# Kernel optimization log

Measured on AMD Instinct MI355X. Metric: run time of the kernel, lower is better.

## Reference

```python
import jax, jax.numpy as jnp
import numpy as np

B, S, FEAT, DK = 128, 2048, 512, 64

def setup_inputs() -> dict:
    key = jax.random.key(0)
    k1, k2, k3, k4, k5 = jax.random.split(key, 5)
    input_k = jax.random.normal(k1, (B, S, FEAT), dtype=jnp.float32)
    input_q = jax.random.normal(k2, (B, FEAT), dtype=jnp.float32)
    context_len = jax.random.randint(k3, (B,), 0, S + 1, dtype=jnp.int32)
    # Linear weights stored as [in, out] so y = x @ W
    W_K = jax.random.normal(k4, (FEAT, DK), dtype=jnp.float32) / np.sqrt(FEAT)
    W_Q = jax.random.normal(k5, (FEAT, DK), dtype=jnp.float32) / np.sqrt(FEAT)
    return {"input_k": input_k, "input_q": input_q, "context_len": context_len,
            "W_K": W_K, "W_Q": W_Q}

def reference(input_k, input_q, context_len, W_K, W_Q):
    # K: [B,S,dk], q: [B,dk]
    K = jnp.einsum('bsf,fd->bsd', input_k, W_K)
    q = input_q @ W_Q
    scores = jnp.einsum('bd,bsd->bs', q, K)  # [B,S] (n_heads=1, no scaling in original)
    mask = jnp.arange(S)[None, :] < context_len[:, None]  # [B,S]
    attn = jax.nn.softmax(jnp.where(mask, scores, -1e30), axis=-1)  # [B,S]
    context = jnp.einsum('bs,bsf->bf', attn, input_k)  # [B,FEAT]
    # length==0 rows produce zeros in the original
    context = jnp.where((context_len > 0)[:, None], context, 0.0)
    return context
```

## Files before the change

### kernel.cpp

```cpp
#include <hip/hip_runtime.h>
#include <math.h>

#define B_    128
#define S_    2048
#define FEAT_ 512
#define DK_   64
#define NSPLIT 32
#define CHUNK  (S_ / NSPLIT)

typedef float f32x4 __attribute__((ext_vector_type(4)));

#define SBAR() __builtin_amdgcn_sched_barrier(0)

__device__ __forceinline__ void ld4(f32x4& d, const float* p) {
  asm volatile("global_load_dwordx4 %0, %1, off" : "=v"(d) : "v"(p) : "memory");
}
__device__ __forceinline__ void ld4o(f32x4& d, const float* p) {
  asm volatile("global_load_dwordx4 %0, %1, off offset:1024"
               : "=v"(d) : "v"(p) : "memory");
}
#define VWAIT(N)                                              \
  do {                                                        \
    asm volatile("s_waitcnt vmcnt(" #N ")" ::: "memory");     \
    SBAR();                                                   \
  } while (0)

#define ISSUE4(d0, d1, d2, d3, d4, d5, d6, d7, srow)                \
  do {                                                              \
    const float* r_ = base + (size_t)(srow) * FEAT_ + lane * 4;     \
    ld4(d0, r_);              ld4o(d1, r_);                         \
    ld4(d2, r_ + 4 * FEAT_);  ld4o(d3, r_ + 4 * FEAT_);             \
    ld4(d4, r_ + 8 * FEAT_);  ld4o(d5, r_ + 8 * FEAT_);             \
    ld4(d6, r_ + 12 * FEAT_); ld4o(d7, r_ + 12 * FEAT_);            \
    SBAR();                                                         \
  } while (0)

__device__ __forceinline__ float dot8(f32x4 x0, f32x4 x1, f32x4 v0, f32x4 v1) {
  float p = x0[0] * v0[0];
  p = fmaf(x0[1], v0[1], p);
  p = fmaf(x0[2], v0[2], p);
  p = fmaf(x0[3], v0[3], p);
  p = fmaf(x1[0], v1[0], p);
  p = fmaf(x1[1], v1[1], p);
  p = fmaf(x1[2], v1[2], p);
  p = fmaf(x1[3], v1[3], p);
  return p;
}

__device__ __forceinline__ float wredsum(float p) {
#pragma unroll
  for (int off = 32; off; off >>= 1) p += __shfl_xor(p, off, 64);
  return p;
}

__device__ __forceinline__ void compute4(
    f32x4 x0, f32x4 x1, f32x4 x2, f32x4 x3,
    f32x4 x4, f32x4 x5, f32x4 x6, f32x4 x7,
    f32x4 v0, f32x4 v1, float& m, float& l, f32x4& a0, f32x4& a1) {
  float p0 = dot8(x0, x1, v0, v1);
  float p1 = dot8(x2, x3, v0, v1);
  float p2 = dot8(x4, x5, v0, v1);
  float p3 = dot8(x6, x7, v0, v1);
  p0 = wredsum(p0);
  p1 = wredsum(p1);
  p2 = wredsum(p2);
  p3 = wredsum(p3);
  float mn = fmaxf(fmaxf(fmaxf(p0, p1), fmaxf(p2, p3)), m);
  float sc = __expf(m - mn);
  float w0 = __expf(p0 - mn), w1 = __expf(p1 - mn);
  float w2 = __expf(p2 - mn), w3 = __expf(p3 - mn);
  l = fmaf(l, sc, (w0 + w1) + (w2 + w3));
#pragma unroll
  for (int j = 0; j < 4; ++j) {
    a0[j] = fmaf(w0, x0[j],
            fmaf(w1, x2[j], fmaf(w2, x4[j], fmaf(w3, x6[j], a0[j] * sc))));
    a1[j] = fmaf(w0, x1[j],
            fmaf(w1, x3[j], fmaf(w2, x5[j], fmaf(w3, x7[j], a1[j] * sc))));
  }
  m = mn;
}

__global__ __launch_bounds__(256) void qv_kernel(
    const float* __restrict__ input_q, const float* __restrict__ W_Q,
    const float* __restrict__ W_K, float* __restrict__ v) {
  int b = blockIdx.x;
  int tid = threadIdx.x;
  __shared__ float xq[FEAT_];
  __shared__ float part[4][DK_];
  __shared__ float qs[DK_];
  for (int f = tid; f < FEAT_; f += 256) xq[f] = input_q[b * FEAT_ + f];
  __syncthreads();
  {
    int d = tid & 63, c = tid >> 6;
    float s = 0.f;
    int f0 = c * 128;
    for (int f = f0; f < f0 + 128; ++f) s = fmaf(xq[f], W_Q[f * DK_ + d], s);
    part[c][d] = s;
  }
  __syncthreads();
  if (tid < DK_)
    qs[tid] = part[0][tid] + part[1][tid] + part[2][tid] + part[3][tid];
  __syncthreads();
  for (int f = tid; f < FEAT_; f += 256) {
    const f32x4* wk = (const f32x4*)(W_K + f * DK_);
    float s = 0.f;
#pragma unroll
    for (int d4 = 0; d4 < DK_ / 4; ++d4) {
      f32x4 w = wk[d4];
      s = fmaf(w[0], qs[d4 * 4 + 0], s);
      s = fmaf(w[1], qs[d4 * 4 + 1], s);
      s = fmaf(w[2], qs[d4 * 4 + 2], s);
      s = fmaf(w[3], qs[d4 * 4 + 3], s);
    }
    v[b * FEAT_ + f] = s;
  }
}

__global__ __launch_bounds__(256) void pass_kernel(
    const float* __restrict__ input_k, const int* __restrict__ ctx,
    const float* __restrict__ v, float* __restrict__ pm,
    float* __restrict__ pl, float* __restrict__ pacc) {
  int split = blockIdx.x;
  int b = blockIdx.y;
  int L = ctx[b];
  int s0 = split * CHUNK;
  int tid = threadIdx.x, wave = tid >> 6, lane = tid & 63;
  int idx = b * NSPLIT + split;

  if (s0 >= L) {
    if (tid == 0) { pm[idx] = -INFINITY; pl[idx] = 0.f; }
    return;
  }

  const float* vb = v + b * FEAT_ + lane * 4;
  f32x4 v0, v1;
  ld4(v0, vb);
  ld4o(v1, vb);
  VWAIT(0);

  float m = -INFINITY, l = 0.f;
  f32x4 a0 = {0.f, 0.f, 0.f, 0.f};
  f32x4 a1 = {0.f, 0.f, 0.f, 0.f};

  const float* base = input_k + (size_t)b * S_ * FEAT_;
  int sb = s0 + wave;

  if (L >= s0 + CHUNK) {
    f32x4 c0, c1, c2, c3, c4, c5, c6, c7;
    f32x4 n0, n1, n2, n3, n4, n5, n6, n7;
    ISSUE4(c0, c1, c2, c3, c4, c5, c6, c7, sb);
    ISSUE4(n0, n1, n2, n3, n4, n5, n6, n7, sb + 16);
    VWAIT(8);
    compute4(c0, c1, c2, c3, c4, c5, c6, c7, v0, v1, m, l, a0, a1);
    ISSUE4(c0, c1, c2, c3, c4, c5, c6, c7, sb + 32);
    VWAIT(8);
    compute4(n0, n1, n2, n3, n4, n5, n6, n7, v0, v1, m, l, a0, a1);
    ISSUE4(n0, n1, n2, n3, n4, n5, n6, n7, sb + 48);
    VWAIT(8);
    compute4(c0, c1, c2, c3, c4, c5, c6, c7, v0, v1, m, l, a0, a1);
    VWAIT(0);
    compute4(n0, n1, n2, n3, n4, n5, n6, n7, v0, v1, m, l, a0, a1);
  } else {
    int s1 = L;
    int s = sb;
    for (; s + 12 < s1; s += 16) {
      const float* r_ = base + (size_t)s * FEAT_ + lane * 4;
      f32x4 x0 = *(const f32x4*)(r_);
      f32x4 x1 = *(const f32x4*)(r_ + 256);
      f32x4 x2 = *(const f32x4*)(r_ + 4 * FEAT_);
      f32x4 x3 = *(const f32x4*)(r_ + 4 * FEAT_ + 256);
      f32x4 x4 = *(const f32x4*)(r_ + 8 * FEAT_);
      f32x4 x5 = *(const f32x4*)(r_ + 8 * FEAT_ + 256);
      f32x4 x6 = *(const f32x4*)(r_ + 12 * FEAT_);
      f32x4 x7 = *(const f32x4*)(r_ + 12 * FEAT_ + 256);
      compute4(x0, x1, x2, x3, x4, x5, x6, x7, v0, v1, m, l, a0, a1);
    }
    for (; s < s1; s += 4) {
      const float* r_ = base + (size_t)s * FEAT_ + lane * 4;
      f32x4 x0 = *(const f32x4*)(r_);
      f32x4 x1 = *(const f32x4*)(r_ + 256);
      float p = wredsum(dot8(x0, x1, v0, v1));
      float mn = fmaxf(m, p);
      float sc = __expf(m - mn);
      float w = __expf(p - mn);
      l = fmaf(l, sc, w);
#pragma unroll
      for (int j = 0; j < 4; ++j) {
        a0[j] = fmaf(w, x0[j], a0[j] * sc);
        a1[j] = fmaf(w, x1[j], a1[j] * sc);
      }
      m = mn;
    }
  }

  __shared__ float sm[4], sl[4];
  __shared__ float sa[4][FEAT_];
  if (lane == 0) { sm[wave] = m; sl[wave] = l; }
  *(f32x4*)&sa[wave][lane * 4] = a0;
  *(f32x4*)&sa[wave][256 + lane * 4] = a1;
  __syncthreads();

  float M = fmaxf(fmaxf(sm[0], sm[1]), fmaxf(sm[2], sm[3]));
  float e0 = __expf(sm[0] - M), e1 = __expf(sm[1] - M);
  float e2 = __expf(sm[2] - M), e3 = __expf(sm[3] - M);
  if (tid == 0) {
    pm[idx] = M;
    pl[idx] = e0 * sl[0] + e1 * sl[1] + e2 * sl[2] + e3 * sl[3];
  }
  for (int f = tid; f < FEAT_; f += 256)
    pacc[(size_t)idx * FEAT_ + f] =
        e0 * sa[0][f] + e1 * sa[1][f] + e2 * sa[2][f] + e3 * sa[3][f];
}

__global__ __launch_bounds__(256) void combine_kernel(
    const float* __restrict__ pm, const float* __restrict__ pl,
    const float* __restrict__ pacc, float* __restrict__ out) {
  int b = blockIdx.x;
  int tid = threadIdx.x;
  __shared__ float e[NSPLIT];
  __shared__ float inv_s;
  if (tid < NSPLIT) {
    float mi = pm[b * NSPLIT + tid];
    float M = mi;
#pragma unroll
    for (int off = 16; off; off >>= 1) M = fmaxf(M, __shfl_xor(M, off, 64));
    float ei = (M == -INFINITY) ? 0.f : __expf(mi - M);
    e[tid] = ei;
    float lw = ei * pl[b * NSPLIT + tid];
#pragma unroll
    for (int off = 16; off; off >>= 1) lw += __shfl_xor(lw, off, 64);
    if (tid == 0) inv_s = (lw > 0.f) ? 1.f / lw : 0.f;
  }
  __syncthreads();
  float inv = inv_s;
  for (int f = tid; f < FEAT_; f += 256) {
    float s = 0.f;
    for (int i = 0; i < NSPLIT; ++i)
      if (e[i] > 0.f)
        s = fmaf(e[i], pacc[((size_t)(b * NSPLIT + i)) * FEAT_ + f], s);
    out[b * FEAT_ + f] = s * inv;
  }
}

extern "C" void kernel_launch(void* const* d_in, const int* in_sizes, int n_in,
                              void* d_out, int out_size, void* d_ws, size_t ws_size,
                              hipStream_t stream) {
  const float* input_k = (const float*)d_in[0];
  const float* input_q = (const float*)d_in[1];
  const int*   ctx     = (const int*)d_in[2];
  const float* W_K     = (const float*)d_in[3];
  const float* W_Q     = (const float*)d_in[4];
  float* out = (float*)d_out;

  char* ws = (char*)d_ws;
  float* v    = (float*)ws;
  float* pm   = (float*)(ws + (size_t)B_ * FEAT_ * sizeof(float));
  float* pl   = pm + B_ * NSPLIT;
  float* pacc = pl + B_ * NSPLIT;

  qv_kernel<<<B_, 256, 0, stream>>>(input_q, W_Q, W_K, v);
  pass_kernel<<<dim3(NSPLIT, B_), 256, 0, stream>>>(input_k, ctx, v, pm, pl, pacc);
  combine_kernel<<<B_, 256, 0, stream>>>(pm, pl, pacc, out);
}
```

Before: 76.06 us.

## Stage key rows through LDS with async global_load_lds double buffering

The full-chunk path now streams key rows into a per-wave double-buffered LDS staging area using global_load_lds instead of inline-asm register loads. Each wave reads two rows at a time from LDS, computes the online softmax update, and refills the buffer while the math runs. The tail path also drops from four to two rows per iteration, and the staging buffer is reused for the cross-wave reduction. The aim is to lower VGPR pressure and overlap memory with compute, at the cost of an extra LDS round trip and more lgkm waits per row pair.

```diff
diff --git a/kernel.cpp b/kernel.cpp
--- a/kernel.cpp
+++ b/kernel.cpp
@@ -11,29 +11,22 @@
 typedef float f32x4 __attribute__((ext_vector_type(4)));
 
 #define SBAR() __builtin_amdgcn_sched_barrier(0)
-
-__device__ __forceinline__ void ld4(f32x4& d, const float* p) {
-  asm volatile("global_load_dwordx4 %0, %1, off" : "=v"(d) : "v"(p) : "memory");
-}
-__device__ __forceinline__ void ld4o(f32x4& d, const float* p) {
-  asm volatile("global_load_dwordx4 %0, %1, off offset:1024"
-               : "=v"(d) : "v"(p) : "memory");
-}
-#define VWAIT(N)                                              \
-  do {                                                        \
-    asm volatile("s_waitcnt vmcnt(" #N ")" ::: "memory");     \
-    SBAR();                                                   \
+#define VWAIT(N)                                                  \
+  do {                                                            \
+    asm volatile("s_waitcnt vmcnt(" #N ")" ::: "memory");         \
+    SBAR();                                                       \
   } while (0)
-
-#define ISSUE4(d0, d1, d2, d3, d4, d5, d6, d7, srow)                \
-  do {                                                              \
-    const float* r_ = base + (size_t)(srow) * FEAT_ + lane * 4;     \
-    ld4(d0, r_);              ld4o(d1, r_);                         \
-    ld4(d2, r_ + 4 * FEAT_);  ld4o(d3, r_ + 4 * FEAT_);             \
-    ld4(d4, r_ + 8 * FEAT_);  ld4o(d5, r_ + 8 * FEAT_);             \
-    ld4(d6, r_ + 12 * FEAT_); ld4o(d7, r_ + 12 * FEAT_);            \
-    SBAR();                                                         \
+#define LWAIT()                                                   \
+  do {                                                            \
+    asm volatile("s_waitcnt lgkmcnt(0)" ::: "memory");            \
+    SBAR();                                                       \
   } while (0)
+
+__device__ __forceinline__ void glds16(const float* g, float* l) {
+  __builtin_amdgcn_global_load_lds(
+      (const __attribute__((address_space(1))) void*)g,
+      (__attribute__((address_space(3))) void*)l, 16, 0, 0);
+}
 
 __device__ __forceinline__ float dot8(f32x4 x0, f32x4 x1, f32x4 v0, f32x4 v1) {
   float p = x0[0] * v0[0];
@@ -53,29 +46,22 @@
   return p;
 }
 
-__device__ __forceinline__ void compute4(
-    f32x4 x0, f32x4 x1, f32x4 x2, f32x4 x3,
-    f32x4 x4, f32x4 x5, f32x4 x6, f32x4 x7,
+__device__ __forceinline__ void math2(
+    f32x4 xA0, f32x4 xA1, f32x4 xB0, f32x4 xB1,
     f32x4 v0, f32x4 v1, float& m, float& l, f32x4& a0, f32x4& a1) {
-  float p0 = dot8(x0, x1, v0, v1);
-  float p1 = dot8(x2, x3, v0, v1);
-  float p2 = dot8(x4, x5, v0, v1);
-  float p3 = dot8(x6, x7, v0, v1);
+  float p0 = dot8(xA0, xA1, v0, v1);
+  float p1 = dot8(xB0, xB1, v0, v1);
   p0 = wredsum(p0);
   p1 = wredsum(p1);
-  p2 = wredsum(p2);
-  p3 = wredsum(p3);
-  float mn = fmaxf(fmaxf(fmaxf(p0, p1), fmaxf(p2, p3)), m);
+  float mn = fmaxf(m, fmaxf(p0, p1));
   float sc = __expf(m - mn);
-  float w0 = __expf(p0 - mn), w1 = __expf(p1 - mn);
-  float w2 = __expf(p2 - mn), w3 = __expf(p3 - mn);
-  l = fmaf(l, sc, (w0 + w1) + (w2 + w3));
+  float w0 = __expf(p0 - mn);
+  float w1 = __expf(p1 - mn);
+  l = fmaf(l, sc, w0 + w1);
 #pragma unroll
   for (int j = 0; j < 4; ++j) {
-    a0[j] = fmaf(w0, x0[j],
-            fmaf(w1, x2[j], fmaf(w2, x4[j], fmaf(w3, x6[j], a0[j] * sc))));
-    a1[j] = fmaf(w0, x1[j],
-            fmaf(w1, x3[j], fmaf(w2, x5[j], fmaf(w3, x7[j], a1[j] * sc))));
+    a0[j] = fmaf(w0, xA0[j], fmaf(w1, xB0[j], a0[j] * sc));
+    a1[j] = fmaf(w0, xA1[j], fmaf(w1, xB1[j], a1[j] * sc));
   }
   m = mn;
 }
@@ -120,6 +106,9 @@
     const float* __restrict__ input_k, const int* __restrict__ ctx,
     const float* __restrict__ v, float* __restrict__ pm,
     float* __restrict__ pl, float* __restrict__ pacc) {
+  __shared__ __align__(16) float stage[4][2][1024];
+  __shared__ float sm[4], sl[4];
+
   int split = blockIdx.x;
   int b = blockIdx.y;
   int L = ctx[b];
@@ -133,49 +122,73 @@
   }
 
   const float* vb = v + b * FEAT_ + lane * 4;
-  f32x4 v0, v1;
-  ld4(v0, vb);
-  ld4o(v1, vb);
-  VWAIT(0);
+  f32x4 v0 = *(const f32x4*)vb;
+  f32x4 v1 = *(const f32x4*)(vb + 256);
 
   float m = -INFINITY, l = 0.f;
   f32x4 a0 = {0.f, 0.f, 0.f, 0.f};
   f32x4 a1 = {0.f, 0.f, 0.f, 0.f};
 
   const float* base = input_k + (size_t)b * S_ * FEAT_;
-  int sb = s0 + wave;
+  float* st0 = &stage[wave][0][0];
+  float* st1 = &stage[wave][1][0];
 
   if (L >= s0 + CHUNK) {
-    f32x4 c0, c1, c2, c3, c4, c5, c6, c7;
-    f32x4 n0, n1, n2, n3, n4, n5, n6, n7;
-    ISSUE4(c0, c1, c2, c3, c4, c5, c6, c7, sb);
-    ISSUE4(n0, n1, n2, n3, n4, n5, n6, n7, sb + 16);
-    VWAIT(8);
-    compute4(c0, c1, c2, c3, c4, c5, c6, c7, v0, v1, m, l, a0, a1);
-    ISSUE4(c0, c1, c2, c3, c4, c5, c6, c7, sb + 32);
-    VWAIT(8);
-    compute4(n0, n1, n2, n3, n4, n5, n6, n7, v0, v1, m, l, a0, a1);
-    ISSUE4(n0, n1, n2, n3, n4, n5, n6, n7, sb + 48);
-    VWAIT(8);
-    compute4(c0, c1, c2, c3, c4, c5, c6, c7, v0, v1, m, l, a0, a1);
+    const float* rb = base + (size_t)(s0 + wave) * FEAT_ + lane * 4;
+#define GISSUE(g_, st_)                                     \
+    do {                                                    \
+      const float* gp_ = rb + (size_t)4096 * (g_);          \
+      glds16(gp_,        (st_));                            \
+      glds16(gp_ + 256,  (st_) + 256);                      \
+      glds16(gp_ + 2048, (st_) + 512);                      \
+      glds16(gp_ + 2304, (st_) + 768);                      \
+    } while (0)
+#define LOAD2(st_, xA0, xA1, xB0, xB1)                      \
+    do {                                                    \
+      const f32x4* p_ = (const f32x4*)(st_) + lane;         \
+      xA0 = p_[0];                                          \
+      xA1 = p_[64];                                         \
+      xB0 = p_[128];                                        \
+      xB1 = p_[192];                                        \
+    } while (0)
+
+    GISSUE(0, st0);
+    GISSUE(1, st1);
     VWAIT(0);
-    compute4(n0, n1, n2, n3, n4, n5, n6, n7, v0, v1, m, l, a0, a1);
+#pragma unroll
+    for (int g = 0; g < 6; ++g) {
+      float* cur = (g & 1) ? st1 : st0;
+      f32x4 xA0, xA1, xB0, xB1;
+      LOAD2(cur, xA0, xA1, xB0, xB1);
+      LWAIT();
+      GISSUE(g + 2, cur);
+      math2(xA0, xA1, xB0, xB1, v0, v1, m, l, a0, a1);
+      VWAIT(4);
+    }
+    {
+      f32x4 xA0, xA1, xB0, xB1;
+      LOAD2(st0, xA0, xA1, xB0, xB1);
+      math2(xA0, xA1, xB0, xB1, v0, v1, m, l, a0, a1);
+    }
+    VWAIT(0);
+    {
+      f32x4 xA0, xA1, xB0, xB1;
+      LOAD2(st1, xA0, xA1, xB0, xB1);
+      math2(xA0, xA1, xB0, xB1, v0, v1, m, l, a0, a1);
+    }
+#undef GISSUE
+#undef LOAD2
   } else {
-    int s1 = L;
-    int s = sb;
-    for (; s + 12 < s1; s += 16) {
+    int s = s0 + wave;
+    for (; s + 4 < L; s += 8) {
       const float* r_ = base + (size_t)s * FEAT_ + lane * 4;
-      f32x4 x0 = *(const f32x4*)(r_);
-      f32x4 x1 = *(const f32x4*)(r_ + 256);
-      f32x4 x2 = *(const f32x4*)(r_ + 4 * FEAT_);
-      f32x4 x3 = *(const f32x4*)(r_ + 4 * FEAT_ + 256);
-      f32x4 x4 = *(const f32x4*)(r_ + 8 * FEAT_);
-      f32x4 x5 = *(const f32x4*)(r_ + 8 * FEAT_ + 256);
-      f32x4 x6 = *(const f32x4*)(r_ + 12 * FEAT_);
-      f32x4 x7 = *(const f32x4*)(r_ + 12 * FEAT_ + 256);
-      compute4(x0, x1, x2, x3, x4, x5, x6, x7, v0, v1, m, l, a0, a1);
-    }
-    for (; s < s1; s += 4) {
+      f32x4 xA0 = *(const f32x4*)(r_);
+      f32x4 xA1 = *(const f32x4*)(r_ + 256);
+      f32x4 xB0 = *(const f32x4*)(r_ + 4 * FEAT_);
+      f32x4 xB1 = *(const f32x4*)(r_ + 4 * FEAT_ + 256);
+      math2(xA0, xA1, xB0, xB1, v0, v1, m, l, a0, a1);
+    }
+    if (s < L) {
       const float* r_ = base + (size_t)s * FEAT_ + lane * 4;
       f32x4 x0 = *(const f32x4*)(r_);
       f32x4 x1 = *(const f32x4*)(r_ + 256);
@@ -193,11 +206,12 @@
     }
   }
 
-  __shared__ float sm[4], sl[4];
-  __shared__ float sa[4][FEAT_];
   if (lane == 0) { sm[wave] = m; sl[wave] = l; }
-  *(f32x4*)&sa[wave][lane * 4] = a0;
-  *(f32x4*)&sa[wave][256 + lane * 4] = a1;
+  {
+    f32x4* sw = (f32x4*)&stage[wave][0][0];
+    sw[lane] = a0;
+    sw[64 + lane] = a1;
+  }
   __syncthreads();
 
   float M = fmaxf(fmaxf(sm[0], sm[1]), fmaxf(sm[2], sm[3]));
@@ -209,7 +223,8 @@
   }
   for (int f = tid; f < FEAT_; f += 256)
     pacc[(size_t)idx * FEAT_ + f] =
-        e0 * sa[0][f] + e1 * sa[1][f] + e2 * sa[2][f] + e3 * sa[3][f];
+        e0 * stage[0][0][f] + e1 * stage[1][0][f] +
+        e2 * stage[2][0][f] + e3 * stage[3][0][f];
 }
 
 __global__ __launch_bounds__(256) void combine_kernel(
```

Result: slower. 78.16 us (+2.8%).

## Interleave sequence rows across splits instead of contiguous chunks per split

Applied to the files above, without the earlier changes.

Each split block now takes rows split, split+NSPLIT, split+2*NSPLIT, ... instead of a contiguous CHUNK of rows. This balances work across splits when context lengths are ragged, so no split carries a full chunk while others idle. The hand-written inline-asm double-buffered load pipeline is removed in favour of a plain compiler-scheduled loop. Strided row access loses contiguity between rows inside a block, and the explicit memory-latency overlap is gone.

```diff
diff --git a/kernel.cpp b/kernel.cpp
--- a/kernel.cpp
+++ b/kernel.cpp
@@ -6,34 +6,9 @@
 #define FEAT_ 512
 #define DK_   64
 #define NSPLIT 32
-#define CHUNK  (S_ / NSPLIT)
+#define RSTRIDE (NSPLIT * FEAT_)
 
 typedef float f32x4 __attribute__((ext_vector_type(4)));
-
-#define SBAR() __builtin_amdgcn_sched_barrier(0)
-
-__device__ __forceinline__ void ld4(f32x4& d, const float* p) {
-  asm volatile("global_load_dwordx4 %0, %1, off" : "=v"(d) : "v"(p) : "memory");
-}
-__device__ __forceinline__ void ld4o(f32x4& d, const float* p) {
-  asm volatile("global_load_dwordx4 %0, %1, off offset:1024"
-               : "=v"(d) : "v"(p) : "memory");
-}
-#define VWAIT(N)                                              \
-  do {                                                        \
-    asm volatile("s_waitcnt vmcnt(" #N ")" ::: "memory");     \
-    SBAR();                                                   \
-  } while (0)
-
-#define ISSUE4(d0, d1, d2, d3, d4, d5, d6, d7, srow)                \
-  do {                                                              \
-    const float* r_ = base + (size_t)(srow) * FEAT_ + lane * 4;     \
-    ld4(d0, r_);              ld4o(d1, r_);                         \
-    ld4(d2, r_ + 4 * FEAT_);  ld4o(d3, r_ + 4 * FEAT_);             \
-    ld4(d4, r_ + 8 * FEAT_);  ld4o(d5, r_ + 8 * FEAT_);             \
-    ld4(d6, r_ + 12 * FEAT_); ld4o(d7, r_ + 12 * FEAT_);            \
-    SBAR();                                                         \
-  } while (0)
 
 __device__ __forceinline__ float dot8(f32x4 x0, f32x4 x1, f32x4 v0, f32x4 v1) {
   float p = x0[0] * v0[0];
@@ -53,33 +28,6 @@
   return p;
 }
 
-__device__ __forceinline__ void compute4(
-    f32x4 x0, f32x4 x1, f32x4 x2, f32x4 x3,
-    f32x4 x4, f32x4 x5, f32x4 x6, f32x4 x7,
-    f32x4 v0, f32x4 v1, float& m, float& l, f32x4& a0, f32x4& a1) {
-  float p0 = dot8(x0, x1, v0, v1);
-  float p1 = dot8(x2, x3, v0, v1);
-  float p2 = dot8(x4, x5, v0, v1);
-  float p3 = dot8(x6, x7, v0, v1);
-  p0 = wredsum(p0);
-  p1 = wredsum(p1);
-  p2 = wredsum(p2);
-  p3 = wredsum(p3);
-  float mn = fmaxf(fmaxf(fmaxf(p0, p1), fmaxf(p2, p3)), m);
-  float sc = __expf(m - mn);
-  float w0 = __expf(p0 - mn), w1 = __expf(p1 - mn);
-  float w2 = __expf(p2 - mn), w3 = __expf(p3 - mn);
-  l = fmaf(l, sc, (w0 + w1) + (w2 + w3));
-#pragma unroll
-  for (int j = 0; j < 4; ++j) {
-    a0[j] = fmaf(w0, x0[j],
-            fmaf(w1, x2[j], fmaf(w2, x4[j], fmaf(w3, x6[j], a0[j] * sc))));
-    a1[j] = fmaf(w0, x1[j],
-            fmaf(w1, x3[j], fmaf(w2, x5[j], fmaf(w3, x7[j], a1[j] * sc))));
-  }
-  m = mn;
-}
-
 __global__ __launch_bounds__(256) void qv_kernel(
     const float* __restrict__ input_q, const float* __restrict__ W_Q,
     const float* __restrict__ W_K, float* __restrict__ v) {
@@ -123,74 +71,74 @@
   int split = blockIdx.x;
   int b = blockIdx.y;
   int L = ctx[b];
-  int s0 = split * CHUNK;
   int tid = threadIdx.x, wave = tid >> 6, lane = tid & 63;
   int idx = b * NSPLIT + split;
 
-  if (s0 >= L) {
+  if (split >= L) {
     if (tid == 0) { pm[idx] = -INFINITY; pl[idx] = 0.f; }
     return;
   }
+  int nt = (L - split + NSPLIT - 1) / NSPLIT;
 
   const float* vb = v + b * FEAT_ + lane * 4;
-  f32x4 v0, v1;
-  ld4(v0, vb);
-  ld4o(v1, vb);
-  VWAIT(0);
+  f32x4 v0 = *(const f32x4*)vb;
+  f32x4 v1 = *(const f32x4*)(vb + 256);
 
   float m = -INFINITY, l = 0.f;
   f32x4 a0 = {0.f, 0.f, 0.f, 0.f};
   f32x4 a1 = {0.f, 0.f, 0.f, 0.f};
 
-  const float* base = input_k + (size_t)b * S_ * FEAT_;
-  int sb = s0 + wave;
-
-  if (L >= s0 + CHUNK) {
-    f32x4 c0, c1, c2, c3, c4, c5, c6, c7;
-    f32x4 n0, n1, n2, n3, n4, n5, n6, n7;
-    ISSUE4(c0, c1, c2, c3, c4, c5, c6, c7, sb);
-    ISSUE4(n0, n1, n2, n3, n4, n5, n6, n7, sb + 16);
-    VWAIT(8);
-    compute4(c0, c1, c2, c3, c4, c5, c6, c7, v0, v1, m, l, a0, a1);
-    ISSUE4(c0, c1, c2, c3, c4, c5, c6, c7, sb + 32);
-    VWAIT(8);
-    compute4(n0, n1, n2, n3, n4, n5, n6, n7, v0, v1, m, l, a0, a1);
-    ISSUE4(n0, n1, n2, n3, n4, n5, n6, n7, sb + 48);
-    VWAIT(8);
-    compute4(c0, c1, c2, c3, c4, c5, c6, c7, v0, v1, m, l, a0, a1);
-    VWAIT(0);
-    compute4(n0, n1, n2, n3, n4, n5, n6, n7, v0, v1, m, l, a0, a1);
-  } else {
-    int s1 = L;
-    int s = sb;
-    for (; s + 12 < s1; s += 16) {
-      const float* r_ = base + (size_t)s * FEAT_ + lane * 4;
-      f32x4 x0 = *(const f32x4*)(r_);
-      f32x4 x1 = *(const f32x4*)(r_ + 256);
-      f32x4 x2 = *(const f32x4*)(r_ + 4 * FEAT_);
-      f32x4 x3 = *(const f32x4*)(r_ + 4 * FEAT_ + 256);
-      f32x4 x4 = *(const f32x4*)(r_ + 8 * FEAT_);
-      f32x4 x5 = *(const f32x4*)(r_ + 8 * FEAT_ + 256);
-      f32x4 x6 = *(const f32x4*)(r_ + 12 * FEAT_);
-      f32x4 x7 = *(const f32x4*)(r_ + 12 * FEAT_ + 256);
-      compute4(x0, x1, x2, x3, x4, x5, x6, x7, v0, v1, m, l, a0, a1);
+  const float* base = input_k + (size_t)b * S_ * FEAT_ + split * FEAT_ + lane * 4;
+
+  int t = wave;
+  for (; t + 12 < nt; t += 16) {
+    const float* r_ = base + (size_t)t * RSTRIDE;
+    f32x4 x0 = *(const f32x4*)(r_);
+    f32x4 x1 = *(const f32x4*)(r_ + 256);
+    f32x4 x2 = *(const f32x4*)(r_ + 4 * (size_t)RSTRIDE);
+    f32x4 x3 = *(const f32x4*)(r_ + 4 * (size_t)RSTRIDE + 256);
+    f32x4 x4 = *(const f32x4*)(r_ + 8 * (size_t)RSTRIDE);
+    f32x4 x5 = *(const f32x4*)(r_ + 8 * (size_t)RSTRIDE + 256);
+    f32x4 x6 = *(const f32x4*)(r_ + 12 * (size_t)RSTRIDE);
+    f32x4 x7 = *(const f32x4*)(r_ + 12 * (size_t)RSTRIDE + 256);
+
+    float p0 = dot8(x0, x1, v0, v1);
+    float p1 = dot8(x2, x3, v0, v1);
+    float p2 = dot8(x4, x5, v0, v1);
+    float p3 = dot8(x6, x7, v0, v1);
+    p0 = wredsum(p0);
+    p1 = wredsum(p1);
+    p2 = wredsum(p2);
+    p3 = wredsum(p3);
+    float mn = fmaxf(fmaxf(fmaxf(p0, p1), fmaxf(p2, p3)), m);
+    float sc = __expf(m - mn);
+    float w0 = __expf(p0 - mn), w1 = __expf(p1 - mn);
+    float w2 = __expf(p2 - mn), w3 = __expf(p3 - mn);
+    l = fmaf(l, sc, (w0 + w1) + (w2 + w3));
+#pragma unroll
+    for (int j = 0; j < 4; ++j) {
+      a0[j] = fmaf(w0, x0[j],
+              fmaf(w1, x2[j], fmaf(w2, x4[j], fmaf(w3, x6[j], a0[j] * sc))));
+      a1[j] = fmaf(w0, x1[j],
+              fmaf(w1, x3[j], fmaf(w2, x5[j], fmaf(w3, x7[j], a1[j] * sc))));
     }
-    for (; s < s1; s += 4) {
-      const float* r_ = base + (size_t)s * FEAT_ + lane * 4;
-      f32x4 x0 = *(const f32x4*)(r_);
-      f32x4 x1 = *(const f32x4*)(r_ + 256);
-      float p = wredsum(dot8(x0, x1, v0, v1));
-      float mn = fmaxf(m, p);
-      float sc = __expf(m - mn);
-      float w = __expf(p - mn);
-      l = fmaf(l, sc, w);
-#pragma unroll
-      for (int j = 0; j < 4; ++j) {
-        a0[j] = fmaf(w, x0[j], a0[j] * sc);
-        a1[j] = fmaf(w, x1[j], a1[j] * sc);
-      }
-      m = mn;
+    m = mn;
+  }
+  for (; t < nt; t += 4) {
+    const float* r_ = base + (size_t)t * RSTRIDE;
+    f32x4 x0 = *(const f32x4*)(r_);
+    f32x4 x1 = *(const f32x4*)(r_ + 256);
+    float p = wredsum(dot8(x0, x1, v0, v1));
+    float mn = fmaxf(m, p);
+    float sc = __expf(m - mn);
+    float w = __expf(p - mn);
+    l = fmaf(l, sc, w);
+#pragma unroll
+    for (int j = 0; j < 4; ++j) {
+      a0[j] = fmaf(w, x0[j], a0[j] * sc);
+      a1[j] = fmaf(w, x1[j], a1[j] * sc);
     }
+    m = mn;
   }
 
   __shared__ float sm[4], sl[4];
```

After: 78.05 us. 2.6% more time.
